# Optimization experiments

Measured on AMD Instinct MI355X. Metric: run time of the kernel, lower is better.

The kernel has to match this reference:

```python
import jax, jax.numpy as jnp
import numpy as np

N_SEG = 128      # number of ragged segments (len(leng))
TOTAL = 32768    # total rows = sum(leng)
D = 1280         # cnn_feature (tf_efficientnet_b0 classifier.in_features)
D_HEAD = 512     # hidden of logits head


def setup_inputs() -> dict:
    key = jax.random.key(0)
    ks = jax.random.split(key, 8)
    # ragged lengths (static at trace time), summing exactly to TOTAL
    rng = np.random.default_rng(0)
    leng = rng.integers(64, 448, size=N_SEG).astype(np.int64)
    leng = np.maximum((leng * (TOTAL / leng.sum())).astype(np.int64), 1)
    leng[-1] += TOTAL - leng.sum()
    segment_ids = jnp.asarray(np.repeat(np.arange(N_SEG), leng), jnp.int32)

    features = jax.random.normal(ks[0], (TOTAL, D), jnp.float32)
    s = 0.02
    Ww = jax.random.normal(ks[1], (D, D), jnp.float32) * s        # proj_w.weight
    bw = jnp.zeros((D,), jnp.float32)                              # proj_w.bias
    v = jax.random.normal(ks[2], (D,), jnp.float32) * s           # proj_v.weight (1,D) squeezed
    W1 = jax.random.normal(ks[3], (D_HEAD, D), jnp.float32) * s   # logits[0].weight
    b1 = jnp.zeros((D_HEAD,), jnp.float32)
    W2 = jax.random.normal(ks[4], (1, D_HEAD), jnp.float32) * s   # logits[3].weight
    b2 = jnp.zeros((1,), jnp.float32)
    return {"features": features, "Ww": Ww, "bw": bw, "v": v,
            "W1": W1, "b1": b1, "W2": W2, "b2": b2,
            "segment_ids": segment_ids}


def reference(features, Ww, bw, v, W1, b1, W2, b2, segment_ids):
    # per-row attention logits: tanh(x @ Ww^T + bw) @ v    -> [TOTAL]
    H = jnp.tanh(features @ Ww.T + bw)
    s = H @ v
    # segment-wise stable softmax (replaces Python loop over leng)
    m = jax.ops.segment_max(s, segment_ids, num_segments=N_SEG)
    e = jnp.exp(s - m[segment_ids])
    z = jax.ops.segment_sum(e, segment_ids, num_segments=N_SEG)
    att = e / z[segment_ids]                                      # [TOTAL]
    # attention-weighted sum pooling per segment -> [N_SEG, D]
    pooled = jax.ops.segment_sum(features * att[:, None], segment_ids,
                                 num_segments=N_SEG)
    # logits head (dropout is identity in eval)
    h = jax.nn.relu(pooled @ W1.T + b1)
    return h @ W2.T + b2                                          # [N_SEG, 1]
```

## Files before the change

### kernel.cpp

```cpp
#include <hip/hip_runtime.h>
#include <hip/hip_bf16.h>


#define TOTAL_ROWS 32768
#define DIM 1280
#define NSEG 128
#define DHEAD 512

typedef _Float16 f16x8 __attribute__((ext_vector_type(8)));
typedef _Float16 f16x4 __attribute__((ext_vector_type(4)));
typedef float f32x4 __attribute__((ext_vector_type(4)));

#define OFF_XH   0
#define OFF_WH   83886080
#define OFF_S    87162880
#define OFF_SEG  87425024
#define OFF_POOL 87426048
#define OFF_H    88081408

__device__ __forceinline__ void load_lds16(const void* g, void* l) {
  __builtin_amdgcn_global_load_lds(
      (const __attribute__((address_space(1))) unsigned int*)g,
      (__attribute__((address_space(3))) unsigned int*)l, 16, 0, 0);
}

__device__ __forceinline__ float tanh_fast(float x) {
  float e = __expf(2.0f * x);
  return 1.0f - 2.0f * __builtin_amdgcn_rcpf(e + 1.0f);
}

__global__ void cvt_init_kernel(const float* __restrict__ a, _Float16* __restrict__ oa,
                                int na8, const float* __restrict__ b,
                                _Float16* __restrict__ ob, int nb8,
                                const int* __restrict__ sid,
                                int* __restrict__ segstart, float* __restrict__ s,
                                float* __restrict__ pooled) {
  int i = blockIdx.x * blockDim.x + threadIdx.x;
  if (i < TOTAL_ROWS) {
    s[i] = 0.f;
    int sg = sid[i];
    if (i == 0) segstart[0] = 0;
    else if (sid[i - 1] != sg) segstart[sg] = i;
    if (i == TOTAL_ROWS - 1) segstart[sg + 1] = TOTAL_ROWS;
  }
  if (i < NSEG * DIM) pooled[i] = 0.f;
  const float* in;
  _Float16* out;
  int idx;
  if (i < na8) {
    in = a; out = oa; idx = i;
  } else {
    idx = i - na8;
    if (idx >= nb8) return;
    in = b; out = ob;
  }
  const float4* p = (const float4*)in + (size_t)idx * 2;
  float4 u0 = p[0], u1 = p[1];
  f16x8 h;
  h[0] = (_Float16)u0.x; h[1] = (_Float16)u0.y;
  h[2] = (_Float16)u0.z; h[3] = (_Float16)u0.w;
  h[4] = (_Float16)u1.x; h[5] = (_Float16)u1.y;
  h[6] = (_Float16)u1.z; h[7] = (_Float16)u1.w;
  *((f16x8*)out + idx) = h;
}

__global__ __launch_bounds__(256) void gemm_s_kernel(
    const _Float16* __restrict__ X, const _Float16* __restrict__ W,
    const float* __restrict__ v, const float* __restrict__ bw,
    float* __restrict__ s) {
  __shared__ _Float16 As[128 * 64];
  __shared__ _Float16 Bs[128 * 64];
  const int rowBase = blockIdx.x * 128;
  const int jBase = blockIdx.y * 128;
  const int t = threadIdx.x;
  const int lane = t & 63;
  const int w = t >> 6;
  const int wm = w & 1, wn = w >> 1;
  const int kc = lane >> 4;
  const int lm = lane & 15;

  int aBase[2], bBase[2];
#pragma unroll
  for (int s2 = 0; s2 < 2; ++s2) {
    int swz = ((kc + s2 * 4 + lm) & 7) * 8;
    aBase[s2] = (wm * 64 + lm) * 64 + swz;
    bBase[s2] = (wn * 64 + lm) * 64 + swz;
  }

  const int subrow = lane >> 3;
  const int g = ((lane & 7) - subrow) & 7;
  const _Float16* gA = X + (size_t)(rowBase + w * 32 + subrow) * DIM + g * 8;
  const _Float16* gB = W + (size_t)(jBase + w * 32 + subrow) * DIM + g * 8;

  f32x4 acc[4][4];
  const f32x4 zero = {0.f, 0.f, 0.f, 0.f};
#pragma unroll
  for (int i = 0; i < 4; ++i)
#pragma unroll
    for (int j = 0; j < 4; ++j) acc[i][j] = zero;

  for (int k0 = 0; k0 < DIM; k0 += 64) {
    __syncthreads();
#pragma unroll
    for (int q = 0; q < 4; ++q) {
      load_lds16(gA + k0 + q * (8 * DIM), &As[(w * 256 + q * 64) * 8]);
      load_lds16(gB + k0 + q * (8 * DIM), &Bs[(w * 256 + q * 64) * 8]);
    }
    __syncthreads();

#pragma unroll
    for (int s2 = 0; s2 < 2; ++s2) {
      f16x8 a[4], b[4];
#pragma unroll
      for (int mt = 0; mt < 4; ++mt) {
        a[mt] = *(const f16x8*)&As[aBase[s2] + mt * 1024];
        b[mt] = *(const f16x8*)&Bs[bBase[s2] + mt * 1024];
      }
#pragma unroll
      for (int mt = 0; mt < 4; ++mt)
#pragma unroll
        for (int nt = 0; nt < 4; ++nt)
          acc[mt][nt] = __builtin_amdgcn_mfma_f32_16x16x32_f16(
              a[mt], b[nt], acc[mt][nt], 0, 0, 0);
    }
  }

  const int colBase = jBase + wn * 64 + lm;
  float vv[4], bb[4];
#pragma unroll
  for (int nt = 0; nt < 4; ++nt) {
    int j = colBase + nt * 16;
    vv[nt] = v[j];
    bb[nt] = bw[j];
  }
  const int gq = lane >> 4;
#pragma unroll
  for (int mt = 0; mt < 4; ++mt) {
#pragma unroll
    for (int r = 0; r < 4; ++r) {
      float sumv = 0.f;
#pragma unroll
      for (int nt = 0; nt < 4; ++nt)
        sumv += tanh_fast(acc[mt][nt][r] + bb[nt]) * vv[nt];
      sumv += __shfl_xor(sumv, 1);
      sumv += __shfl_xor(sumv, 2);
      sumv += __shfl_xor(sumv, 4);
      sumv += __shfl_xor(sumv, 8);
      if (lm == 0) {
        int row = rowBase + wm * 64 + mt * 16 + gq * 4 + r;
        atomicAdd(&s[row], sumv);
      }
    }
  }
}

__global__ void softpool_kernel(const _Float16* __restrict__ F,
                                const float* __restrict__ s,
                                const int* __restrict__ segstart,
                                float* __restrict__ pooled) {
  int seg = blockIdx.x, part = blockIdx.y;
  int st = segstart[seg], en = segstart[seg + 1];
  int t = threadIdx.x;
  __shared__ float redm[5], redz[5];
  float m = -1e30f;
  for (int i = st + t; i < en; i += 320) m = fmaxf(m, s[i]);
  for (int d = 1; d < 64; d <<= 1) m = fmaxf(m, __shfl_xor(m, d));
  if ((t & 63) == 0) redm[t >> 6] = m;
  __syncthreads();
  m = fmaxf(fmaxf(fmaxf(redm[0], redm[1]), fmaxf(redm[2], redm[3])), redm[4]);
  float z = 0.f;
  for (int i = st + t; i < en; i += 320) z += __expf(s[i] - m);
  for (int d = 1; d < 64; d <<= 1) z += __shfl_xor(z, d);
  if ((t & 63) == 0) redz[t >> 6] = z;
  __syncthreads();
  z = redz[0] + redz[1] + redz[2] + redz[3] + redz[4];
  float rz = 1.0f / z;

  int len = en - st;
  int chunk = (len + 7) >> 3;
  int r0 = st + chunk * part;
  int r1 = min(en, r0 + chunk);
  float acc[4] = {0.f, 0.f, 0.f, 0.f};
  int r = r0;
  for (; r + 2 <= r1; r += 2) {
    float a0 = __expf(s[r] - m) * rz;
    float a1 = __expf(s[r + 1] - m) * rz;
    f16x4 f0 = ((const f16x4*)(F + (size_t)r * DIM))[t];
    f16x4 f1 = ((const f16x4*)(F + (size_t)(r + 1) * DIM))[t];
#pragma unroll
    for (int c = 0; c < 4; ++c) {
      acc[c] = fmaf(a0, (float)f0[c], acc[c]);
      acc[c] = fmaf(a1, (float)f1[c], acc[c]);
    }
  }
  if (r < r1) {
    float a0 = __expf(s[r] - m) * rz;
    f16x4 f0 = ((const f16x4*)(F + (size_t)r * DIM))[t];
#pragma unroll
    for (int c = 0; c < 4; ++c) acc[c] = fmaf(a0, (float)f0[c], acc[c]);
  }
  float* dst = pooled + (size_t)seg * DIM + t * 4;
#pragma unroll
  for (int c = 0; c < 4; ++c) atomicAdd(dst + c, acc[c]);
}

__global__ void head1_kernel(const float* __restrict__ pooled,
                             const float* __restrict__ W1,
                             const float* __restrict__ b1, float* __restrict__ h) {
  int og = blockIdx.x, sg = blockIdx.y;
  __shared__ float Wt[16 * 65];
  __shared__ float Pt[32 * 65];
  int t = threadIdx.x;
  int tx = t & 15, ty = t >> 4;
  float acc0 = 0.f, acc1 = 0.f;
  for (int kcc = 0; kcc < 20; ++kcc) {
    __syncthreads();
#pragma unroll
    for (int u = 0; u < 4; ++u) {
      int lin = t + 256 * u;
      int o = lin >> 6, kk = lin & 63;
      Wt[o * 65 + kk] = W1[(size_t)(og * 16 + o) * DIM + kcc * 64 + kk];
    }
#pragma unroll
    for (int u = 0; u < 8; ++u) {
      int lin = t + 256 * u;
      int ss = lin >> 6, kk = lin & 63;
      Pt[ss * 65 + kk] = pooled[(size_t)(sg * 32 + ss) * DIM + kcc * 64 + kk];
    }
    __syncthreads();
#pragma unroll
    for (int kk = 0; kk < 64; ++kk) {
      float wv = Wt[tx * 65 + kk];
      acc0 = fmaf(Pt[ty * 65 + kk], wv, acc0);
      acc1 = fmaf(Pt[(ty + 16) * 65 + kk], wv, acc1);
    }
  }
  int o = og * 16 + tx;
  float bias = b1[o];
  h[(size_t)(sg * 32 + ty) * DHEAD + o] = fmaxf(acc0 + bias, 0.f);
  h[(size_t)(sg * 32 + ty + 16) * DHEAD + o] = fmaxf(acc1 + bias, 0.f);
}

__global__ void head2_kernel(const float* __restrict__ h,
                             const float* __restrict__ W2,
                             const float* __restrict__ b2, float* __restrict__ out) {
  int seg = blockIdx.x;
  int t = threadIdx.x;
  float val = h[(size_t)seg * DHEAD + t] * W2[t] +
              h[(size_t)seg * DHEAD + t + 256] * W2[t + 256];
  for (int d = 1; d < 64; d <<= 1) val += __shfl_xor(val, d);
  __shared__ float red[4];
  if ((t & 63) == 0) red[t >> 6] = val;
  __syncthreads();
  if (t == 0) out[seg] = red[0] + red[1] + red[2] + red[3] + b2[0];
}

extern "C" void kernel_launch(void* const* d_in, const int* in_sizes, int n_in,
                              void* d_out, int out_size, void* d_ws, size_t ws_size,
                              hipStream_t stream) {
  const float* features = (const float*)d_in[0];
  const float* Ww = (const float*)d_in[1];
  const float* bw = (const float*)d_in[2];
  const float* v = (const float*)d_in[3];
  const float* W1 = (const float*)d_in[4];
  const float* b1 = (const float*)d_in[5];
  const float* W2 = (const float*)d_in[6];
  const float* b2 = (const float*)d_in[7];
  const int* segids = (const int*)d_in[8];
  float* out = (float*)d_out;

  char* ws = (char*)d_ws;
  _Float16* Xh = (_Float16*)(ws + OFF_XH);
  _Float16* Wh = (_Float16*)(ws + OFF_WH);
  float* s = (float*)(ws + OFF_S);
  int* segstart = (int*)(ws + OFF_SEG);
  float* pooled = (float*)(ws + OFF_POOL);
  float* h = (float*)(ws + OFF_H);

  const int na8 = TOTAL_ROWS * DIM / 8;
  const int nb8 = DIM * DIM / 8;
  cvt_init_kernel<<<(na8 + nb8 + 255) / 256, 256, 0, stream>>>(
      features, Xh, na8, Ww, Wh, nb8, segids, segstart, s, pooled);

  dim3 ggrid(TOTAL_ROWS / 128, DIM / 128);
  gemm_s_kernel<<<ggrid, 256, 0, stream>>>(Xh, Wh, v, bw, s);

  softpool_kernel<<<dim3(NSEG, 8), 320, 0, stream>>>(Xh, s, segstart, pooled);
  head1_kernel<<<dim3(32, 4), 256, 0, stream>>>(pooled, W1, b1, h);
  head2_kernel<<<NSEG, 256, 0, stream>>>(h, W2, b2, out);
}
```

Measured before the change: 474.8 us.

## Rewrite score GEMM as 256x256 double-buffered tiles with phased MFMA/load overlap

```diff
diff --git a/kernel.cpp b/kernel.cpp
--- a/kernel.cpp
+++ b/kernel.cpp
@@ -6,6 +6,7 @@
 #define DIM 1280
 #define NSEG 128
 #define DHEAD 512
+#define NKT 20
 
 typedef _Float16 f16x8 __attribute__((ext_vector_type(8)));
 typedef _Float16 f16x4 __attribute__((ext_vector_type(4)));
@@ -64,66 +65,127 @@
   *((f16x8*)out + idx) = h;
 }
 
-__global__ __launch_bounds__(256) void gemm_s_kernel(
+__global__ __launch_bounds__(512, 2) void gemm_s_kernel(
     const _Float16* __restrict__ X, const _Float16* __restrict__ W,
     const float* __restrict__ v, const float* __restrict__ bw,
     float* __restrict__ s) {
-  __shared__ _Float16 As[128 * 64];
-  __shared__ _Float16 Bs[128 * 64];
-  const int rowBase = blockIdx.x * 128;
-  const int jBase = blockIdx.y * 128;
+  __shared__ _Float16 As[2][2][8192];
+  __shared__ _Float16 Bs[2][2][8192];
+
+  const int rowBase = blockIdx.x * 256;
+  const int jBase = blockIdx.y * 256;
   const int t = threadIdx.x;
   const int lane = t & 63;
   const int w = t >> 6;
-  const int wm = w & 1, wn = w >> 1;
+  const int wm = w >> 2;
+  const int wn = w & 3;
+  const int lm = lane & 15;
   const int kc = lane >> 4;
-  const int lm = lane & 15;
-
-  int aBase[2], bBase[2];
-#pragma unroll
-  for (int s2 = 0; s2 < 2; ++s2) {
-    int swz = ((kc + s2 * 4 + lm) & 7) * 8;
-    aBase[s2] = (wm * 64 + lm) * 64 + swz;
-    bBase[s2] = (wn * 64 + lm) * 64 + swz;
-  }
+  const int bh = wn >> 1;
 
   const int subrow = lane >> 3;
   const int g = ((lane & 7) - subrow) & 7;
-  const _Float16* gA = X + (size_t)(rowBase + w * 32 + subrow) * DIM + g * 8;
-  const _Float16* gB = W + (size_t)(jBase + w * 32 + subrow) * DIM + g * 8;
-
-  f32x4 acc[4][4];
+  const _Float16* gA = X + (size_t)(rowBase + w * 8 + subrow) * DIM + g * 8;
+  const _Float16* gB = W + (size_t)(jBase + w * 8 + subrow) * DIM + g * 8;
+
+  int aOff[2], bOff[2];
+#pragma unroll
+  for (int ks = 0; ks < 2; ++ks) {
+    int swz = ((ks * 4 + kc + lm) & 7) * 8;
+    aOff[ks] = lm * 64 + swz;
+    bOff[ks] = ((wn & 1) * 64 + lm) * 64 + swz;
+  }
+
+  f32x4 acc[8][4];
   const f32x4 zero = {0.f, 0.f, 0.f, 0.f};
 #pragma unroll
-  for (int i = 0; i < 4; ++i)
+  for (int i = 0; i < 8; ++i)
 #pragma unroll
     for (int j = 0; j < 4; ++j) acc[i][j] = zero;
 
-  for (int k0 = 0; k0 < DIM; k0 += 64) {
-    __syncthreads();
-#pragma unroll
-    for (int q = 0; q < 4; ++q) {
-      load_lds16(gA + k0 + q * (8 * DIM), &As[(w * 256 + q * 64) * 8]);
-      load_lds16(gB + k0 + q * (8 * DIM), &Bs[(w * 256 + q * 64) * 8]);
-    }
-    __syncthreads();
-
-#pragma unroll
-    for (int s2 = 0; s2 < 2; ++s2) {
-      f16x8 a[4], b[4];
-#pragma unroll
-      for (int mt = 0; mt < 4; ++mt) {
-        a[mt] = *(const f16x8*)&As[aBase[s2] + mt * 1024];
-        b[mt] = *(const f16x8*)&Bs[bBase[s2] + mt * 1024];
-      }
-#pragma unroll
-      for (int mt = 0; mt < 4; ++mt)
-#pragma unroll
-        for (int nt = 0; nt < 4; ++nt)
-          acc[mt][nt] = __builtin_amdgcn_mfma_f32_16x16x32_f16(
-              a[mt], b[nt], acc[mt][nt], 0, 0, 0);
-    }
-  }
+  f16x8 a[4][2], b[2][2];
+
+#define STAGE_A(BUF, HALF, TT) do { \
+    const _Float16* _src = gA + (size_t)(HALF) * 128 * DIM + (size_t)(TT) * 64; \
+    load_lds16(_src, &As[BUF][HALF][w * 512]); \
+    load_lds16(_src + 64 * DIM, &As[BUF][HALF][4096 + w * 512]); \
+  } while (0)
+#define STAGE_B(BUF, HALF, TT) do { \
+    const _Float16* _src = gB + (size_t)(HALF) * 128 * DIM + (size_t)(TT) * 64; \
+    load_lds16(_src, &Bs[BUF][HALF][w * 512]); \
+    load_lds16(_src + 64 * DIM, &Bs[BUF][HALF][4096 + w * 512]); \
+  } while (0)
+
+#define PH_READ_A(BUF, MTB) do { \
+    _Pragma("unroll") for (int mt = 0; mt < 4; ++mt) \
+    _Pragma("unroll") for (int ks = 0; ks < 2; ++ks) \
+      a[mt][ks] = *(const f16x8*)&As[BUF][wm][aOff[ks] + (MTB + mt) * 1024]; \
+  } while (0)
+#define PH_READ_B(BUF, NTB) do { \
+    _Pragma("unroll") for (int nt = 0; nt < 2; ++nt) \
+    _Pragma("unroll") for (int ks = 0; ks < 2; ++ks) \
+      b[nt][ks] = *(const f16x8*)&Bs[BUF][bh][bOff[ks] + (NTB + nt) * 1024]; \
+  } while (0)
+#define PH_MFMA(MTB, NTB) do { \
+    __builtin_amdgcn_s_setprio(1); \
+    _Pragma("unroll") for (int mt = 0; mt < 4; ++mt) \
+    _Pragma("unroll") for (int nt = 0; nt < 2; ++nt) \
+    _Pragma("unroll") for (int ks = 0; ks < 2; ++ks) \
+      acc[MTB + mt][NTB + nt] = __builtin_amdgcn_mfma_f32_16x16x32_f16( \
+          a[mt][ks], b[nt][ks], acc[MTB + mt][NTB + nt], 0, 0, 0); \
+    __builtin_amdgcn_s_setprio(0); \
+  } while (0)
+
+#define CFENCE asm volatile("" ::: "memory")
+#define LGKM0  asm volatile("s_waitcnt lgkmcnt(0)" ::: "memory")
+#define WAIT_VM4 asm volatile("s_waitcnt vmcnt(4)" ::: "memory")
+#define WAIT_VM0 asm volatile("s_waitcnt vmcnt(0)" ::: "memory")
+#define BAR __builtin_amdgcn_s_barrier()
+
+#define KTILE(BUF, S0, S1, S3, TAILWAIT) do { \
+    CFENCE; \
+     \
+    PH_READ_A(BUF, 0); PH_READ_B(BUF, 0); S0; \
+    BAR; LGKM0; PH_MFMA(0, 0); BAR; \
+     \
+    PH_READ_B(BUF, 2); S1; \
+    BAR; LGKM0; PH_MFMA(0, 2); BAR; \
+     \
+    PH_READ_A(BUF, 4); PH_READ_B(BUF, 0); \
+    BAR; LGKM0; PH_MFMA(4, 0); BAR; \
+     \
+    PH_READ_B(BUF, 2); S3; \
+    BAR; LGKM0; PH_MFMA(4, 2); \
+    TAILWAIT; BAR; \
+  } while (0)
+
+  STAGE_A(0, 0, 0); STAGE_A(0, 1, 0);
+  STAGE_B(0, 0, 0); STAGE_B(0, 1, 0);
+  STAGE_A(1, 0, 1); STAGE_A(1, 1, 1);
+  WAIT_VM4;
+  BAR;
+
+  for (int kt = 0; kt < NKT - 2; kt += 2) {
+    KTILE(0,
+          STAGE_B(1, 0, kt + 1),
+          STAGE_B(1, 1, kt + 1),
+          { STAGE_A(0, 0, kt + 2); STAGE_A(0, 1, kt + 2); },
+          WAIT_VM4);
+    KTILE(1,
+          STAGE_B(0, 0, kt + 2),
+          STAGE_B(0, 1, kt + 2),
+          { STAGE_A(1, 0, kt + 3); STAGE_A(1, 1, kt + 3); },
+          WAIT_VM4);
+  }
+  KTILE(0, STAGE_B(1, 0, NKT - 1), STAGE_B(1, 1, NKT - 1), (void)0, WAIT_VM0);
+  KTILE(1, (void)0, (void)0, (void)0, (void)0);
+
+#undef KTILE
+#undef STAGE_A
+#undef STAGE_B
+#undef PH_READ_A
+#undef PH_READ_B
+#undef PH_MFMA
 
   const int colBase = jBase + wn * 64 + lm;
   float vv[4], bb[4];
@@ -135,7 +197,7 @@
   }
   const int gq = lane >> 4;
 #pragma unroll
-  for (int mt = 0; mt < 4; ++mt) {
+  for (int mt = 0; mt < 8; ++mt) {
 #pragma unroll
     for (int r = 0; r < 4; ++r) {
       float sumv = 0.f;
@@ -147,7 +209,7 @@
       sumv += __shfl_xor(sumv, 4);
       sumv += __shfl_xor(sumv, 8);
       if (lm == 0) {
-        int row = rowBase + wm * 64 + mt * 16 + gq * 4 + r;
+        int row = rowBase + wm * 128 + mt * 16 + gq * 4 + r;
         atomicAdd(&s[row], sumv);
       }
     }
@@ -282,8 +344,8 @@
   cvt_init_kernel<<<(na8 + nb8 + 255) / 256, 256, 0, stream>>>(
       features, Xh, na8, Ww, Wh, nb8, segids, segstart, s, pooled);
 
-  dim3 ggrid(TOTAL_ROWS / 128, DIM / 128);
-  gemm_s_kernel<<<ggrid, 256, 0, stream>>>(Xh, Wh, v, bw, s);
+  dim3 ggrid(TOTAL_ROWS / 256, DIM / 256);
+  gemm_s_kernel<<<ggrid, 512, 0, stream>>>(Xh, Wh, v, bw, s);
 
   softpool_kernel<<<dim3(NSEG, 8), 320, 0, stream>>>(Xh, s, segstart, pooled);
   head1_kernel<<<dim3(32, 4), 256, 0, stream>>>(pooled, W1, b1, h);
```

Measured after the change: 482.9 us. No clear change (+1.7%).
